# Optimization experiments

Hardware: AMD Instinct MI355X
Metric: run time of the kernel (lower is better)

The kernel has to match this reference:

```python
import jax, jax.numpy as jnp
import numpy as np

D_IN = 2048
NUM_LATENTS = 32768
K = 32
B, S = 2, 2048


def setup_inputs() -> dict:
    key = jax.random.key(0)
    k1, k2 = jax.random.split(key)
    x = jax.random.normal(k1, (B, S, D_IN), dtype=jnp.float32)
    # encoder: nn.Linear(d_in, num_latents) -> weight [num_latents, d_in]
    W_enc = jax.random.normal(k2, (NUM_LATENTS, D_IN), dtype=jnp.float32) / np.sqrt(D_IN)
    b_enc = jnp.zeros((NUM_LATENTS,), dtype=jnp.float32)  # bias zeroed in __init__
    # W_dec initialized as encoder weight clone, rows normalized to unit norm
    norm = jnp.linalg.norm(W_enc, axis=1, keepdims=True)
    W_dec = W_enc / (norm + 1e-5)
    b_dec = jnp.zeros((D_IN,), dtype=jnp.float32)
    return {"x": x, "W_enc": W_enc, "b_enc": b_enc, "W_dec": W_dec, "b_dec": b_dec}


def reference(x, W_enc, b_enc, W_dec, b_dec):
    # encode: linear on centered input, then top-k over latent dim
    pre = jnp.einsum('bsd,ld->bsl', x - b_dec, W_enc) + b_enc  # [B,S,L]
    top_acts, top_idx = jax.lax.top_k(pre, K)                  # [B,S,K]
    # decode: weighted sum of selected decoder rows (embedding_bag mode='sum')
    rows = jnp.take(W_dec, top_idx, axis=0)                    # [B,S,K,D]
    x_hat = jnp.einsum('bsk,bskd->bsd', top_acts, rows) + b_dec
    return x_hat
```

## Files before the change

### kernel.cpp

```cpp
#include <hip/hip_runtime.h>
#include <hip/hip_bf16.h>
#include <stdint.h>

typedef unsigned short u16;
typedef __attribute__((ext_vector_type(8))) short short8;
typedef __attribute__((ext_vector_type(4))) float f32x4;
typedef __attribute__((ext_vector_type(8))) unsigned short u16x8;

#define D_INK 2048
#define NLAT  32768
#define NTOK  4096
#define TOPK  32
#define CANDMAX 192

__device__ __forceinline__ u16 f2bf(float f) {
  __hip_bfloat16 h = __float2bfloat16(f);
  u16 u; __builtin_memcpy(&u, &h, 2); return u;
}

__device__ __forceinline__ void load_lds16(const u16* g, u16* l) {
  __builtin_amdgcn_global_load_lds(
      (const __attribute__((address_space(1))) unsigned int*)g,
      (__attribute__((address_space(3))) unsigned int*)l, 16, 0, 0);
}

__global__ __launch_bounds__(256) void convert_w_kernel(const float* __restrict__ in, u16* __restrict__ out) {
  size_t i = ((size_t)blockIdx.x * 256 + threadIdx.x) * 8;
  float4 a = *reinterpret_cast<const float4*>(in + i);
  float4 b = *reinterpret_cast<const float4*>(in + i + 4);
  u16x8 o;
  o[0]=f2bf(a.x); o[1]=f2bf(a.y); o[2]=f2bf(a.z); o[3]=f2bf(a.w);
  o[4]=f2bf(b.x); o[5]=f2bf(b.y); o[6]=f2bf(b.z); o[7]=f2bf(b.w);
  *reinterpret_cast<u16x8*>(out + i) = o;
}

__global__ __launch_bounds__(256) void convert_x_kernel(const float* __restrict__ x, const float* __restrict__ b_dec,
                                                        u16* __restrict__ out) {
  size_t i = ((size_t)blockIdx.x * 256 + threadIdx.x) * 8;
  int d = (int)(i & (D_INK - 1));
  float4 a = *reinterpret_cast<const float4*>(x + i);
  float4 b = *reinterpret_cast<const float4*>(x + i + 4);
  float4 ba = *reinterpret_cast<const float4*>(b_dec + d);
  float4 bb = *reinterpret_cast<const float4*>(b_dec + d + 4);
  u16x8 o;
  o[0]=f2bf(a.x-ba.x); o[1]=f2bf(a.y-ba.y); o[2]=f2bf(a.z-ba.z); o[3]=f2bf(a.w-ba.w);
  o[4]=f2bf(b.x-bb.x); o[5]=f2bf(b.y-bb.y); o[6]=f2bf(b.z-bb.z); o[7]=f2bf(b.w-bb.w);
  *reinterpret_cast<u16x8*>(out + i) = o;
}

__global__ __launch_bounds__(256) void gemm_kernel(
    const u16* __restrict__ A,
    const u16* __restrict__ B,
    const float* __restrict__ b_enc,
    u16* __restrict__ pre,
    int tokBase, int tokTiles)
{
  __shared__ alignas(16) u16 As[128 * 64];
  __shared__ alignas(16) u16 Bs[128 * 64];
  const int tokTile = blockIdx.x % tokTiles;
  const int latTile = blockIdx.x / tokTiles;
  const int tid  = threadIdx.x;
  const int wave = tid >> 6, lane = tid & 63;
  const int wm = wave >> 1, wn = wave & 1;
  const int rloc = lane >> 3, cswz = lane & 7;
  const int cdat = cswz ^ rloc;
  const int m16 = lane & 15, quad = lane >> 4;

  const int rowA0 = tokBase + tokTile * 128;
  const int rowB0 = latTile * 128;

  f32x4 acc[4][4];
  #pragma unroll
  for (int i = 0; i < 4; ++i)
    #pragma unroll
    for (int j = 0; j < 4; ++j) { acc[i][j][0]=0.f; acc[i][j][1]=0.f; acc[i][j][2]=0.f; acc[i][j][3]=0.f; }

  for (int kt = 0; kt < D_INK / 64; ++kt) {
    const int k0 = kt * 64;
    #pragma unroll
    for (int i = 0; i < 4; ++i) {
      const int seg = wave * 4 + i;
      const u16* ga = A + (size_t)(rowA0 + seg * 8 + rloc) * D_INK + k0 + cdat * 8;
      load_lds16(ga, &As[seg * 64 * 8]);
      const u16* gb = B + (size_t)(rowB0 + seg * 8 + rloc) * D_INK + k0 + cdat * 8;
      load_lds16(gb, &Bs[seg * 64 * 8]);
    }
    __syncthreads();
    #pragma unroll
    for (int ks = 0; ks < 2; ++ks) {
      short8 af[4], bf[4];
      #pragma unroll
      for (int mi = 0; mi < 4; ++mi) {
        const int r = wm * 64 + mi * 16 + m16;
        const int ci = r * 8 + ((ks * 4 + quad) ^ (r & 7));
        af[mi] = *reinterpret_cast<const short8*>(&As[ci * 8]);
      }
      #pragma unroll
      for (int ni = 0; ni < 4; ++ni) {
        const int r = wn * 64 + ni * 16 + m16;
        const int ci = r * 8 + ((ks * 4 + quad) ^ (r & 7));
        bf[ni] = *reinterpret_cast<const short8*>(&Bs[ci * 8]);
      }
      #pragma unroll
      for (int mi = 0; mi < 4; ++mi)
        #pragma unroll
        for (int ni = 0; ni < 4; ++ni)
          acc[mi][ni] = __builtin_amdgcn_mfma_f32_16x16x32_bf16(af[mi], bf[ni], acc[mi][ni], 0, 0, 0);
    }
    __syncthreads();
  }

  #pragma unroll
  for (int ni = 0; ni < 4; ++ni) {
    const int col = latTile * 128 + wn * 64 + ni * 16 + m16;
    const float be = b_enc[col];
    #pragma unroll
    for (int mi = 0; mi < 4; ++mi) {
      const int row = tokTile * 128 + wm * 64 + mi * 16 + quad * 4;
      #pragma unroll
      for (int r = 0; r < 4; ++r)
        pre[(size_t)(row + r) * NLAT + col] = f2bf(acc[mi][ni][r] + be);
    }
  }
}

__global__ __launch_bounds__(256, 8) void topk_decode_kernel(
    const u16* __restrict__ pre, const float* __restrict__ x,
    const float* __restrict__ W_enc, const float* __restrict__ b_enc,
    const float* __restrict__ W_dec, const float* __restrict__ b_dec,
    float* __restrict__ out, int tokBase)
{
  __shared__ int   hist[1024];
  __shared__ alignas(16) float xs[D_INK];
  __shared__ int   candIdx[CANDMAX];
  __shared__ float candVal[CANDMAX];
  __shared__ int   candCount;
  __shared__ int   tauBin;
  __shared__ float selVal[TOPK];
  __shared__ int   selIdx[TOPK];

  const int tid = threadIdx.x;
  const int lane = tid & 63, wave = tid >> 6;
  const int t = tokBase + blockIdx.x;

  for (int i = tid; i < 1024; i += 256) hist[i] = 0;
  if (tid == 0) candCount = 0;
  for (int i = tid; i < D_INK; i += 256) xs[i] = x[(size_t)t * D_INK + i] - b_dec[i];
  __syncthreads();

  const uint4* prow = reinterpret_cast<const uint4*>(pre + (size_t)blockIdx.x * NLAT);
  for (int it = 0; it < NLAT / (256 * 8); ++it) {
    uint4 v = prow[it * 256 + tid];
    unsigned w[4] = {v.x, v.y, v.z, v.w};
    #pragma unroll
    for (int j = 0; j < 4; ++j) {
      unsigned lo = w[j] & 0xFFFFu, hi = w[j] >> 16;
      unsigned klo = (lo & 0x8000u) ? (0xFFFFu ^ lo) : (lo | 0x8000u);
      unsigned khi = (hi & 0x8000u) ? (0xFFFFu ^ hi) : (hi | 0x8000u);
      if (klo >= 0xC000u) atomicAdd(&hist[(klo >> 4) - 3072], 1);
      if (khi >= 0xC000u) atomicAdd(&hist[(khi >> 4) - 3072], 1);
    }
  }
  __syncthreads();
  if (wave == 0) {
    const int g = 63 - lane;
    int c = 0;
    #pragma unroll
    for (int j = 0; j < 16; ++j) c += hist[g * 16 + j];
    int p = c;
    #pragma unroll
    for (int off = 1; off < 64; off <<= 1) {
      int v = __shfl_up(p, off);
      if (lane >= off) p += v;
    }
    unsigned long long m = __ballot(p >= 64);
    int tb;
    if (m == 0ull) {
      tb = 3072;
    } else {
      const int fl = __ffsll((unsigned long long)m) - 1;
      const int cumAbove = __shfl(p - c, fl);
      const int gb = 63 - fl;
      int h = (lane < 16) ? hist[gb * 16 + 15 - lane] : 0;
      int q = h;
      #pragma unroll
      for (int off = 1; off < 16; off <<= 1) {
        int v = __shfl_up(q, off);
        if (lane >= off) q += v;
      }
      unsigned long long m2 = __ballot(lane < 16 && (cumAbove + q) >= 64);
      const int fl2 = __ffsll((unsigned long long)m2) - 1;
      tb = 3072 + gb * 16 + 15 - fl2;
    }
    if (lane == 0) tauBin = tb;
  }
  __syncthreads();
  const int tb = tauBin;
  for (int it = 0; it < NLAT / (256 * 8); ++it) {
    uint4 v = prow[it * 256 + tid];
    const int base = (it * 256 + tid) * 8;
    unsigned w[4] = {v.x, v.y, v.z, v.w};
    #pragma unroll
    for (int j = 0; j < 4; ++j) {
      unsigned lo = w[j] & 0xFFFFu, hi = w[j] >> 16;
      unsigned klo = (lo & 0x8000u) ? (0xFFFFu ^ lo) : (lo | 0x8000u);
      unsigned khi = (hi & 0x8000u) ? (0xFFFFu ^ hi) : (hi | 0x8000u);
      if ((int)(klo >> 4) >= tb) { int p = atomicAdd(&candCount, 1); if (p < CANDMAX) candIdx[p] = base + 2 * j; }
      if ((int)(khi >> 4) >= tb) { int p = atomicAdd(&candCount, 1); if (p < CANDMAX) candIdx[p] = base + 2 * j + 1; }
    }
  }
  __syncthreads();
  const int C = min(candCount, CANDMAX);
  for (int c = wave; c < C; c += 4) {
    const int li = candIdx[c];
    const float2* wr = reinterpret_cast<const float2*>(W_enc + (size_t)li * D_INK);
    const float2* xp = reinterpret_cast<const float2*>(xs);
    double s0 = 0.0, s1 = 0.0;
    #pragma unroll 8
    for (int i = 0; i < D_INK / 128; ++i) {
      const int p = lane + i * 64;
      const float2 w2 = wr[p];
      const float2 x2 = xp[p];
      s0 += (double)x2.x * (double)w2.x;
      s1 += (double)x2.y * (double)w2.y;
    }
    double s = s0 + s1;
    for (int off = 32; off > 0; off >>= 1) s += __shfl_down(s, off);
    if (lane == 0) candVal[c] = (float)(s + (double)b_enc[li]);
  }
  __syncthreads();
  if (wave == 0) {
    float v0[3]; int s0[3]; int ix[3];
    #pragma unroll
    for (int j = 0; j < 3; ++j) {
      const int c = lane + j * 64;
      if (c < C) { v0[j] = candVal[c]; s0[j] = c; ix[j] = candIdx[c]; }
      else       { v0[j] = -1e30f;     s0[j] = -1; ix[j] = 0x7FFFFFFF; }
    }
    for (int r = 0; r < TOPK; ++r) {
      float bv = v0[0]; int bi = ix[0], bs = s0[0];
      #pragma unroll
      for (int j = 1; j < 3; ++j)
        if (v0[j] > bv || (v0[j] == bv && ix[j] < bi)) { bv = v0[j]; bi = ix[j]; bs = s0[j]; }
      for (int off = 32; off > 0; off >>= 1) {
        float ov = __shfl_down(bv, off); int oi = __shfl_down(bi, off); int os = __shfl_down(bs, off);
        if (ov > bv || (ov == bv && oi < bi)) { bv = ov; bi = oi; bs = os; }
      }
      bv = __shfl(bv, 0); bi = __shfl(bi, 0); bs = __shfl(bs, 0);
      if (lane == 0) {
        if (bv <= -1e29f) { selVal[r] = 0.0f; selIdx[r] = 0; }
        else              { selVal[r] = bv;   selIdx[r] = bi; }
      }
      #pragma unroll
      for (int j = 0; j < 3; ++j) if (s0[j] == bs) v0[j] = -1e30f;
    }
  }
  __syncthreads();
  for (int d0 = tid * 4; d0 < D_INK; d0 += 1024) {
    float4 acc = *reinterpret_cast<const float4*>(b_dec + d0);
    #pragma unroll 8
    for (int k = 0; k < TOPK; ++k) {
      const float a = selVal[k];
      const float4 w = *reinterpret_cast<const float4*>(W_dec + (size_t)selIdx[k] * D_INK + d0);
      acc.x += a * w.x; acc.y += a * w.y; acc.z += a * w.z; acc.w += a * w.w;
    }
    *reinterpret_cast<float4*>(out + (size_t)t * D_INK + d0) = acc;
  }
}

extern "C" void kernel_launch(void* const* d_in, const int* in_sizes, int n_in,
                              void* d_out, int out_size, void* d_ws, size_t ws_size,
                              hipStream_t stream) {
  const float* x     = (const float*)d_in[0];
  const float* W_enc = (const float*)d_in[1];
  const float* b_enc = (const float*)d_in[2];
  const float* W_dec = (const float*)d_in[3];
  const float* b_dec = (const float*)d_in[4];
  float* out = (float*)d_out;

  const size_t WHI_BYTES = (size_t)NLAT * D_INK * 2;
  const size_t XHI_BYTES = (size_t)NTOK * D_INK * 2;
  u16* Whi = (u16*)d_ws;
  u16* Xhi = (u16*)((char*)d_ws + WHI_BYTES);
  u16* pre = (u16*)((char*)d_ws + WHI_BYTES + XHI_BYTES);

  size_t preAvail = ws_size > (WHI_BYTES + XHI_BYTES) ? ws_size - WHI_BYTES - XHI_BYTES : 0;
  int Tc = (int)(preAvail / ((size_t)NLAT * 2));
  if (Tc > NTOK) Tc = NTOK;
  Tc = (Tc / 128) * 128;
  if (Tc < 128) Tc = 128;

  convert_w_kernel<<<(NLAT * D_INK / 8) / 256, 256, 0, stream>>>(W_enc, Whi);
  convert_x_kernel<<<(NTOK * D_INK / 8) / 256, 256, 0, stream>>>(x, b_dec, Xhi);

  for (int tokBase = 0; tokBase < NTOK; tokBase += Tc) {
    const int ct = (NTOK - tokBase) < Tc ? (NTOK - tokBase) : Tc;
    const int tokTiles = ct / 128;
    gemm_kernel<<<tokTiles * (NLAT / 128), 256, 0, stream>>>(Xhi, Whi, b_enc, pre, tokBase, tokTiles);
    topk_decode_kernel<<<ct, 256, 0, stream>>>(pre, x, W_enc, b_enc, W_dec, b_dec, out, tokBase);
  }
}
```

Baseline: 2.033 ms.

## Enlarge GEMM tiles to 256x256 with double-buffered LDS and coalesced epilogue

The encoder GEMM moves from 128x128 tiles with 256 threads to 256x256 tiles with 512 threads, which raises arithmetic intensity per tile loaded. The K loop is now double-buffered: the next K slab is prefetched with global_load_lds while the current one computes, synchronised by vmcnt waits and raw barriers. Blocks are remapped in an XCD-aware order, and MFMA sections are raised in priority with s_setprio. The output is staged through LDS so it can be written to `pre` as coalesced 16-byte stores. In exchange it uses 128KB of LDS, which allows only one block per CU, and relies on hand-placed waitcnt and barriers being correct.

```diff
diff --git a/kernel.cpp b/kernel.cpp
--- a/kernel.cpp
+++ b/kernel.cpp
@@ -48,80 +48,116 @@
   *reinterpret_cast<u16x8*>(out + i) = o;
 }
 
-__global__ __launch_bounds__(256) void gemm_kernel(
+__global__ __launch_bounds__(512, 2) void gemm_kernel(
     const u16* __restrict__ A,
     const u16* __restrict__ B,
     const float* __restrict__ b_enc,
     u16* __restrict__ pre,
     int tokBase, int tokTiles)
 {
-  __shared__ alignas(16) u16 As[128 * 64];
-  __shared__ alignas(16) u16 Bs[128 * 64];
-  const int tokTile = blockIdx.x % tokTiles;
-  const int latTile = blockIdx.x / tokTiles;
+  __shared__ alignas(16) u16 sh[65536];
   const int tid  = threadIdx.x;
   const int wave = tid >> 6, lane = tid & 63;
-  const int wm = wave >> 1, wn = wave & 1;
+  const int wm = wave >> 2, wn = wave & 3;
   const int rloc = lane >> 3, cswz = lane & 7;
   const int cdat = cswz ^ rloc;
   const int m16 = lane & 15, quad = lane >> 4;
 
-  const int rowA0 = tokBase + tokTile * 128;
-  const int rowB0 = latTile * 128;
-
-  f32x4 acc[4][4];
+  int bid = blockIdx.x;
+  const int nwg = tokTiles * (NLAT / 256);
+  if ((nwg & 7) == 0) { const int cpx = nwg >> 3; bid = (bid & 7) * cpx + (bid >> 3); }
+  const int tokTile = bid % tokTiles;
+  const int latTile = bid / tokTiles;
+
+  const int rowA0 = tokBase + tokTile * 256;
+  const int rowB0 = latTile * 256;
+
+  f32x4 acc[8][4];
   #pragma unroll
-  for (int i = 0; i < 4; ++i)
+  for (int i = 0; i < 8; ++i)
     #pragma unroll
     for (int j = 0; j < 4; ++j) { acc[i][j][0]=0.f; acc[i][j][1]=0.f; acc[i][j][2]=0.f; acc[i][j][3]=0.f; }
 
-  for (int kt = 0; kt < D_INK / 64; ++kt) {
-    const int k0 = kt * 64;
-    #pragma unroll
-    for (int i = 0; i < 4; ++i) {
-      const int seg = wave * 4 + i;
-      const u16* ga = A + (size_t)(rowA0 + seg * 8 + rloc) * D_INK + k0 + cdat * 8;
-      load_lds16(ga, &As[seg * 64 * 8]);
-      const u16* gb = B + (size_t)(rowB0 + seg * 8 + rloc) * D_INK + k0 + cdat * 8;
-      load_lds16(gb, &Bs[seg * 64 * 8]);
-    }
-    __syncthreads();
-    #pragma unroll
-    for (int ks = 0; ks < 2; ++ks) {
-      short8 af[4], bf[4];
+  #define STAGE(kt_) do {                                                          \
+    const int buf_ = ((kt_) & 1) << 15;                                            \
+    const int k0_  = (kt_) << 6;                                                   \
+    _Pragma("unroll")                                                              \
+    for (int i_ = 0; i_ < 4; ++i_) {                                               \
+      const int seg_ = wave * 4 + i_;                                              \
+      load_lds16(A + (size_t)(rowA0 + seg_ * 8 + rloc) * D_INK + k0_ + cdat * 8,   \
+                 &sh[buf_ + seg_ * 512]);                                          \
+      load_lds16(B + (size_t)(rowB0 + seg_ * 8 + rloc) * D_INK + k0_ + cdat * 8,   \
+                 &sh[buf_ + 16384 + seg_ * 512]);                                  \
+    }                                                                              \
+  } while (0)
+
+  #define COMPUTE(kt_) do {                                                        \
+    const int buf_ = ((kt_) & 1) << 15;                                            \
+    _Pragma("unroll")                                                              \
+    for (int ks_ = 0; ks_ < 2; ++ks_) {                                            \
+      short8 af_[8], bf_[4];                                                       \
+      _Pragma("unroll")                                                            \
+      for (int mi_ = 0; mi_ < 8; ++mi_) {                                          \
+        const int r_ = wm * 128 + mi_ * 16 + m16;                                  \
+        const int ci_ = r_ * 8 + ((ks_ * 4 + quad) ^ (r_ & 7));                    \
+        af_[mi_] = *reinterpret_cast<const short8*>(&sh[buf_ + ci_ * 8]);          \
+      }                                                                            \
+      _Pragma("unroll")                                                            \
+      for (int ni_ = 0; ni_ < 4; ++ni_) {                                          \
+        const int r_ = wn * 64 + ni_ * 16 + m16;                                   \
+        const int ci_ = r_ * 8 + ((ks_ * 4 + quad) ^ (r_ & 7));                    \
+        bf_[ni_] = *reinterpret_cast<const short8*>(&sh[buf_ + 16384 + ci_ * 8]);  \
+      }                                                                            \
+      __builtin_amdgcn_s_setprio(1);                                               \
+      _Pragma("unroll")                                                            \
+      for (int mi_ = 0; mi_ < 8; ++mi_)                                            \
+        _Pragma("unroll")                                                          \
+        for (int ni_ = 0; ni_ < 4; ++ni_)                                          \
+          acc[mi_][ni_] = __builtin_amdgcn_mfma_f32_16x16x32_bf16(                 \
+              af_[mi_], bf_[ni_], acc[mi_][ni_], 0, 0, 0);                         \
+      __builtin_amdgcn_s_setprio(0);                                               \
+    }                                                                              \
+  } while (0)
+
+  STAGE(0);
+  for (int kt = 0; kt < D_INK / 64 - 1; ++kt) {
+    STAGE(kt + 1);
+    asm volatile("s_waitcnt vmcnt(8)" ::: "memory");
+    __builtin_amdgcn_s_barrier();
+    asm volatile("" ::: "memory");
+    COMPUTE(kt);
+    asm volatile("" ::: "memory");
+    __builtin_amdgcn_s_barrier();
+  }
+  asm volatile("s_waitcnt vmcnt(0)" ::: "memory");
+  __builtin_amdgcn_s_barrier();
+  asm volatile("" ::: "memory");
+  COMPUTE(D_INK / 64 - 1);
+  __syncthreads();
+
+  float be[4];
+  #pragma unroll
+  for (int ni = 0; ni < 4; ++ni) be[ni] = b_enc[latTile * 256 + wn * 64 + ni * 16 + m16];
+  #pragma unroll
+  for (int mi = 0; mi < 8; ++mi)
+    #pragma unroll
+    for (int ni = 0; ni < 4; ++ni)
       #pragma unroll
-      for (int mi = 0; mi < 4; ++mi) {
-        const int r = wm * 64 + mi * 16 + m16;
-        const int ci = r * 8 + ((ks * 4 + quad) ^ (r & 7));
-        af[mi] = *reinterpret_cast<const short8*>(&As[ci * 8]);
+      for (int r = 0; r < 4; ++r) {
+        const int row = wm * 128 + mi * 16 + quad * 4 + r;
+        const int col = wn * 64 + ni * 16 + m16;
+        sh[row * 256 + col] = f2bf(acc[mi][ni][r] + be[ni]);
       }
-      #pragma unroll
-      for (int ni = 0; ni < 4; ++ni) {
-        const int r = wn * 64 + ni * 16 + m16;
-        const int ci = r * 8 + ((ks * 4 + quad) ^ (r & 7));
-        bf[ni] = *reinterpret_cast<const short8*>(&Bs[ci * 8]);
-      }
-      #pragma unroll
-      for (int mi = 0; mi < 4; ++mi)
-        #pragma unroll
-        for (int ni = 0; ni < 4; ++ni)
-          acc[mi][ni] = __builtin_amdgcn_mfma_f32_16x16x32_bf16(af[mi], bf[ni], acc[mi][ni], 0, 0, 0);
-    }
-    __syncthreads();
-  }
-
+  __syncthreads();
   #pragma unroll
-  for (int ni = 0; ni < 4; ++ni) {
-    const int col = latTile * 128 + wn * 64 + ni * 16 + m16;
-    const float be = b_enc[col];
-    #pragma unroll
-    for (int mi = 0; mi < 4; ++mi) {
-      const int row = tokTile * 128 + wm * 64 + mi * 16 + quad * 4;
-      #pragma unroll
-      for (int r = 0; r < 4; ++r)
-        pre[(size_t)(row + r) * NLAT + col] = f2bf(acc[mi][ni][r] + be);
-    }
-  }
+  for (int i = 0; i < 16; ++i) {
+    const int idx = i * 512 + tid;
+    const int row = idx >> 5, c = idx & 31;
+    *reinterpret_cast<u16x8*>(pre + (size_t)(tokTile * 256 + row) * NLAT + latTile * 256 + c * 8)
+        = *reinterpret_cast<const u16x8*>(&sh[idx * 8]);
+  }
+  #undef STAGE
+  #undef COMPUTE
 }
 
 __global__ __launch_bounds__(256, 8) void topk_decode_kernel(
@@ -287,16 +323,16 @@
   size_t preAvail = ws_size > (WHI_BYTES + XHI_BYTES) ? ws_size - WHI_BYTES - XHI_BYTES : 0;
   int Tc = (int)(preAvail / ((size_t)NLAT * 2));
   if (Tc > NTOK) Tc = NTOK;
-  Tc = (Tc / 128) * 128;
-  if (Tc < 128) Tc = 128;
+  Tc = (Tc / 256) * 256;
+  if (Tc < 256) Tc = 256;
 
   convert_w_kernel<<<(NLAT * D_INK / 8) / 256, 256, 0, stream>>>(W_enc, Whi);
   convert_x_kernel<<<(NTOK * D_INK / 8) / 256, 256, 0, stream>>>(x, b_dec, Xhi);
 
   for (int tokBase = 0; tokBase < NTOK; tokBase += Tc) {
     const int ct = (NTOK - tokBase) < Tc ? (NTOK - tokBase) : Tc;
-    const int tokTiles = ct / 128;
-    gemm_kernel<<<tokTiles * (NLAT / 128), 256, 0, stream>>>(Xhi, Whi, b_enc, pre, tokBase, tokTiles);
+    const int tokTiles = ct / 256;
+    gemm_kernel<<<tokTiles * (NLAT / 256), 512, 0, stream>>>(Xhi, Whi, b_enc, pre, tokBase, tokTiles);
     topk_decode_kernel<<<ct, 256, 0, stream>>>(pre, x, W_enc, b_enc, W_dec, b_dec, out, tokBase);
   }
 }
```

New measurement: 1.815 ms. 1.12x faster.
